# Kernel optimization log

Hardware: AMD Instinct MI355X
Metric: run time of the kernel (lower is better)

The kernel has to match this reference:

```python
import jax, jax.numpy as jnp
import numpy as np

DIM = 1024
N_HEADS = 16
HEAD_DIM = DIM // N_HEADS


def setup_inputs() -> dict:
    key = jax.random.key(0)
    ks = jax.random.split(key, 9)
    s = 0.02
    return {
        "x": jax.random.normal(ks[0], (2, 2048, DIM), dtype=jnp.float32),
        "Wq": jax.random.normal(ks[1], (DIM, DIM), dtype=jnp.float32) * s,
        "bq": jax.random.normal(ks[2], (DIM,), dtype=jnp.float32) * s,
        "Wk": jax.random.normal(ks[3], (DIM, DIM), dtype=jnp.float32) * s,
        "bk": jax.random.normal(ks[4], (DIM,), dtype=jnp.float32) * s,
        "Wv": jax.random.normal(ks[5], (DIM, DIM), dtype=jnp.float32) * s,
        "bv": jax.random.normal(ks[6], (DIM,), dtype=jnp.float32) * s,
        "Wo": jax.random.normal(ks[7], (DIM, DIM), dtype=jnp.float32) * s,
        "bo": jax.random.normal(ks[8], (DIM,), dtype=jnp.float32) * s,
    }


def reference(x, Wq, bq, Wk, bk, Wv, bv, Wo, bo):
    B, T, C = x.shape
    # QKV projections, split heads -> [B, H, T, D]
    def split_heads(t):
        return t.reshape(B, T, N_HEADS, HEAD_DIM).transpose(0, 2, 1, 3)
    q = split_heads(x @ Wq + bq)
    k = split_heads(x @ Wk + bk)
    v = split_heads(x @ Wv + bv)
    scale = 1.0 / jnp.sqrt(jnp.float32(HEAD_DIM))
    scores = jnp.einsum("bhqd,bhkd->bhqk", q, k) * scale  # [B,H,T,T]
    causal = jnp.tril(jnp.ones((T, T), dtype=bool))  # True = keep
    scores = jnp.where(causal, scores, jnp.float32(-jnp.inf))
    weights = jax.nn.softmax(scores, axis=-1)
    ctx = jnp.einsum("bhqk,bhkd->bhqd", weights, v)
    ctx = ctx.transpose(0, 2, 1, 3).reshape(B, T, C)
    return ctx @ Wo + bo
```

## Files before the change

kernel.cpp:

```cpp
#include <hip/hip_runtime.h>
#include <hip/hip_bf16.h>
#include <stdint.h>

#define DIM    1024
#define SEQ    2048
#define NB     2
#define NH     16
#define HD     64
#define NROWS  (NB*SEQ)

typedef unsigned short u16;
typedef __attribute__((ext_vector_type(8))) short bf16x8;
typedef __attribute__((ext_vector_type(4))) float f32x4;
typedef __attribute__((ext_vector_type(4))) unsigned short u16x4;

#define NEG_INF (-__builtin_inff())

__device__ __forceinline__ u16 f2bf(float f) {
    union { float f; uint32_t u; } x; x.f = f;
    uint32_t r = x.u + 0x7FFFu + ((x.u >> 16) & 1u);
    return (u16)(r >> 16);
}

__device__ __forceinline__ void gload_lds16(const void* g, void* l) {
    __builtin_amdgcn_global_load_lds(
        (const __attribute__((address_space(1))) void*)g,
        (__attribute__((address_space(3))) void*)l, 16, 0, 0);
}

__global__ __launch_bounds__(256)
void cvt_x(const float* __restrict__ in, u16* __restrict__ out)
{
    size_t i = (size_t)blockIdx.x * 256 + threadIdx.x;
    float4 f = *(const float4*)&in[i * 4];
    u16x4 o = { f2bf(f.x), f2bf(f.y), f2bf(f.z), f2bf(f.w) };
    *(u16x4*)&out[i * 4] = o;
}

__global__ __launch_bounds__(256)
void cvt_w(const float* __restrict__ Wq, const float* __restrict__ Wk,
           const float* __restrict__ Wv, const float* __restrict__ Wo,
           u16* __restrict__ Wqt, u16* __restrict__ Wkt,
           u16* __restrict__ Wvt, u16* __restrict__ Wot)
{
    __shared__ u16 Ws[64][68];
    const int z = blockIdx.z;
    const float* W = z == 0 ? Wq : z == 1 ? Wk : z == 2 ? Wv : Wo;
    u16* Wt        = z == 0 ? Wqt : z == 1 ? Wkt : z == 2 ? Wvt : Wot;
    const int k0 = blockIdx.x * 64;
    const int n0 = blockIdx.y * 64;
    const int tid = threadIdx.x;

    #pragma unroll
    for (int it = 0; it < 4; ++it) {
        int idx = tid + it * 256;
        int r = idx >> 4, cq = idx & 15;
        float4 f = *(const float4*)&W[(size_t)(k0 + r) * DIM + n0 + cq * 4];
        u16x4 o = { f2bf(f.x), f2bf(f.y), f2bf(f.z), f2bf(f.w) };
        *(u16x4*)&Ws[r][cq * 4] = o;
    }
    __syncthreads();
    #pragma unroll
    for (int it = 0; it < 4; ++it) {
        int idx = tid + it * 256;
        int rr = idx >> 4, cq = idx & 15;
        u16x4 o = { Ws[cq*4+0][rr], Ws[cq*4+1][rr], Ws[cq*4+2][rr], Ws[cq*4+3][rr] };
        *(u16x4*)&Wt[(size_t)(n0 + rr) * DIM + k0 + cq * 4] = o;
    }
}

template<int MODE>
__global__ __launch_bounds__(256)
void gemm_mfma(const u16* __restrict__ A,
               const u16* __restrict__ Wt0, const u16* __restrict__ Wt1,
               const u16* __restrict__ Wt2,
               const float* __restrict__ b0, const float* __restrict__ b1,
               const float* __restrict__ b2,
               void* __restrict__ o0, void* __restrict__ o1, void* __restrict__ o2)
{
    __shared__ __align__(16) uint8_t lds[32768];
    uint8_t* Asb = lds;
    uint8_t* Bsb = lds + 16384;

    const int tid  = threadIdx.x;
    const int wid  = tid >> 6, lane = tid & 63;
    const int lr   = lane & 15, lg = lane >> 4;
    const int wr   = wid >> 1, wc = wid & 1;

    const int r0 = blockIdx.x * 128;
    const int c0 = blockIdx.y * 128;

    const u16* Wt; const float* bias; u16* obf = nullptr; float* ofp = nullptr;
    int cw;
    if (MODE == 0) {
        int sel = c0 >> 10;
        cw  = c0 & 1023;
        Wt   = sel == 0 ? Wt0 : sel == 1 ? Wt1 : Wt2;
        bias = sel == 0 ? b0  : sel == 1 ? b1  : b2;
        obf  = (u16*)(sel == 0 ? o0 : sel == 1 ? o1 : o2);
    } else {
        cw = c0; Wt = Wt0; bias = b0; ofp = (float*)o0;
    }

    f32x4 acc[4][4] = {};

    for (int k0 = 0; k0 < DIM; k0 += 64) {
        __syncthreads();
        #pragma unroll
        for (int seg = 0; seg < 4; ++seg) {
            int o   = seg * 4096 + tid * 16;
            int row = o >> 7;
            int sch = ((o >> 4) & 7) ^ (row & 7);
            gload_lds16((const uint8_t*)A  + ((size_t)(r0 + row) << 11) + (k0 << 1) + (sch << 4),
                        Asb + seg * 4096 + (wid << 10) + (lane << 4));
            gload_lds16((const uint8_t*)Wt + ((size_t)(cw + row) << 11) + (k0 << 1) + (sch << 4),
                        Bsb + seg * 4096 + (wid << 10) + (lane << 4));
        }
        __syncthreads();

        __builtin_amdgcn_s_setprio(1);
        #pragma unroll
        for (int kk = 0; kk < 2; ++kk) {
            bf16x8 a[4], b[4];
            #pragma unroll
            for (int i = 0; i < 4; ++i) {
                int ar = wr * 64 + i * 16 + lr;
                a[i] = *(const bf16x8*)(Asb + ar * 128 + ((((kk << 2) | lg) ^ (ar & 7)) << 4));
                int br = wc * 64 + i * 16 + lr;
                b[i] = *(const bf16x8*)(Bsb + br * 128 + ((((kk << 2) | lg) ^ (br & 7)) << 4));
            }
            #pragma unroll
            for (int i = 0; i < 4; ++i)
                #pragma unroll
                for (int j = 0; j < 4; ++j)
                    acc[i][j] = __builtin_amdgcn_mfma_f32_16x16x32_bf16(a[i], b[j], acc[i][j], 0, 0, 0);
        }
        __builtin_amdgcn_s_setprio(0);
    }

    #pragma unroll
    for (int j = 0; j < 4; ++j) {
        int colw = wc * 64 + j * 16 + lr;
        float bv = bias[cw + colw];
        #pragma unroll
        for (int i = 0; i < 4; ++i) {
            #pragma unroll
            for (int r = 0; r < 4; ++r) {
                float val = acc[i][j][r] + bv;
                int row = r0 + wr * 64 + i * 16 + lg * 4 + r;
                if (MODE == 0) {
                    int col = cw + colw;
                    int h = col >> 6, d = col & 63;
                    int bb = row >> 11, t = row & (SEQ - 1);
                    obf[((((size_t)bb * NH + h) * SEQ + t) << 6) + d] = f2bf(val);
                } else {
                    ofp[((size_t)row << 10) + c0 + colw] = val;
                }
            }
        }
    }
}

__global__ __launch_bounds__(256)
void attn_mfma(const u16* __restrict__ q, const u16* __restrict__ k,
               const u16* __restrict__ v, u16* __restrict__ ctx)
{
    __shared__ __align__(16) uint8_t lds[32768];
    uint8_t* Qs = lds;
    uint8_t* Ks = lds + 8192;
    uint8_t* Vt = lds + 16384;
    uint8_t* Ps = lds + 24576;

    const int tid = threadIdx.x;
    const int wid = tid >> 6, lane = tid & 63;
    const int lr  = lane & 15, lg = lane >> 4;

    const int n  = blockIdx.x;
    const int j4 = n >> 8;
    const int c  = n & 255;
    const int ch = c >> 5;
    const int bh = c & 31;
    const int qt = (j4 == 0) ? ch : (j4 == 1) ? (15 - ch)
                 : (j4 == 2) ? (16 + ch) : (31 - ch);

    const size_t hb = (size_t)bh * SEQ * HD;
    const int q0 = qt * 64;

    #pragma unroll
    for (int seg = 0; seg < 2; ++seg) {
        int o = seg * 4096 + tid * 16;
        int row = o >> 7;
        int sch = ((o >> 4) & 7) ^ (row & 7);
        gload_lds16((const uint8_t*)(q + hb) + (size_t)(q0 + row) * 128 + (sch << 4),
                    Qs + seg * 4096 + (wid << 10) + (lane << 4));
    }

    const int vp = tid >> 3;
    const int vg = tid & 7;

    f32x4 acc[4] = {};
    float mrow[4] = {NEG_INF, NEG_INF, NEG_INF, NEG_INF};
    float lrow[4] = {0.f, 0.f, 0.f, 0.f};
    bf16x8 aQ0, aQ1;

    for (int kt = 0; kt <= qt; ++kt) {
        __syncthreads();
        #pragma unroll
        for (int seg = 0; seg < 2; ++seg) {
            int o = seg * 4096 + tid * 16;
            int row = o >> 7;
            int sch = ((o >> 4) & 7) ^ (row & 7);
            gload_lds16((const uint8_t*)(k + hb) + (size_t)(kt * 64 + row) * 128 + (sch << 4),
                        Ks + seg * 4096 + (wid << 10) + (lane << 4));
        }
        {
            const u16* vsrc = v + hb + ((size_t)(kt * 64 + 2 * vp) << 6) + vg * 8;
            bf16x8 v0 = *(const bf16x8*)vsrc;
            bf16x8 v1 = *(const bf16x8*)(vsrc + 64);
            #pragma unroll
            for (int i = 0; i < 8; ++i) {
                int d = vg * 8 + i;
                int swzd = (d ^ (d >> 3)) & 7;
                uint32_t w = (uint32_t)(u16)v0[i] | ((uint32_t)(u16)v1[i] << 16);
                *(uint32_t*)(Vt + d * 128 + ((((vp >> 2) ^ swzd) << 4)) + ((vp & 3) << 2)) = w;
            }
        }
        __syncthreads();

        if (kt == 0) {
            int qr = wid * 16 + lr;
            aQ0 = *(const bf16x8*)(Qs + qr * 128 + ((lg       ^ (qr & 7)) << 4));
            aQ1 = *(const bf16x8*)(Qs + qr * 128 + (((4 | lg) ^ (qr & 7)) << 4));
        }

        f32x4 s[4];
        __builtin_amdgcn_s_setprio(1);
        #pragma unroll
        for (int j = 0; j < 4; ++j) {
            int krow = j * 16 + lr;
            bf16x8 b0 = *(const bf16x8*)(Ks + krow * 128 + ((lg       ^ (krow & 7)) << 4));
            bf16x8 b1 = *(const bf16x8*)(Ks + krow * 128 + (((4 | lg) ^ (krow & 7)) << 4));
            f32x4 z = {0.f, 0.f, 0.f, 0.f};
            z    = __builtin_amdgcn_mfma_f32_16x16x32_bf16(aQ0, b0, z, 0, 0, 0);
            s[j] = __builtin_amdgcn_mfma_f32_16x16x32_bf16(aQ1, b1, z, 0, 0, 0);
        }
        __builtin_amdgcn_s_setprio(0);

        #pragma unroll
        for (int j = 0; j < 4; ++j)
            #pragma unroll
            for (int r = 0; r < 4; ++r)
                s[j][r] *= 0.125f;
        if (kt == qt) {
            #pragma unroll
            for (int j = 0; j < 4; ++j) {
                int kcol = j * 16 + lr;
                #pragma unroll
                for (int r = 0; r < 4; ++r)
                    if (kcol > wid * 16 + lg * 4 + r) s[j][r] = NEG_INF;
            }
        }

        float alpha[4];
        #pragma unroll
        for (int r = 0; r < 4; ++r) {
            float rm = fmaxf(fmaxf(s[0][r], s[1][r]), fmaxf(s[2][r], s[3][r]));
            rm = fmaxf(rm, __shfl_xor(rm, 1));
            rm = fmaxf(rm, __shfl_xor(rm, 2));
            rm = fmaxf(rm, __shfl_xor(rm, 4));
            rm = fmaxf(rm, __shfl_xor(rm, 8));
            float mn = fmaxf(mrow[r], rm);
            alpha[r] = __expf(mrow[r] - mn);
            mrow[r] = mn;
        }
        float rs[4] = {0.f, 0.f, 0.f, 0.f};
        #pragma unroll
        for (int j = 0; j < 4; ++j)
            #pragma unroll
            for (int r = 0; r < 4; ++r) {
                float p = __expf(s[j][r] - mrow[r]);
                s[j][r] = p;
                rs[r] += p;
            }
        #pragma unroll
        for (int r = 0; r < 4; ++r) {
            float t = rs[r];
            t += __shfl_xor(t, 1);
            t += __shfl_xor(t, 2);
            t += __shfl_xor(t, 4);
            t += __shfl_xor(t, 8);
            lrow[r] = lrow[r] * alpha[r] + t;
        }

        #pragma unroll
        for (int j = 0; j < 4; ++j)
            #pragma unroll
            for (int r = 0; r < 4; ++r) {
                int row = wid * 16 + lg * 4 + r;
                int swzp = (row ^ (row >> 2)) & 7;
                int col = j * 16 + lr;
                *(u16*)(Ps + row * 128 + ((((col >> 3) ^ swzp) << 4)) + ((col & 7) << 1))
                    = f2bf(s[j][r]);
            }

        #pragma unroll
        for (int ni = 0; ni < 4; ++ni)
            #pragma unroll
            for (int r = 0; r < 4; ++r)
                acc[ni][r] *= alpha[r];

        int prow = wid * 16 + lr;
        int swzq = (prow ^ (prow >> 2)) & 7;
        bf16x8 pa0 = *(const bf16x8*)(Ps + prow * 128 + ((lg       ^ swzq) << 4));
        bf16x8 pa1 = *(const bf16x8*)(Ps + prow * 128 + (((4 | lg) ^ swzq) << 4));
        __builtin_amdgcn_s_setprio(1);
        #pragma unroll
        for (int ni = 0; ni < 4; ++ni) {
            int vrow = ni * 16 + lr;
            int swzd = (vrow ^ (vrow >> 3)) & 7;
            bf16x8 vb0 = *(const bf16x8*)(Vt + vrow * 128 + ((lg       ^ swzd) << 4));
            bf16x8 vb1 = *(const bf16x8*)(Vt + vrow * 128 + (((4 | lg) ^ swzd) << 4));
            acc[ni] = __builtin_amdgcn_mfma_f32_16x16x32_bf16(pa0, vb0, acc[ni], 0, 0, 0);
            acc[ni] = __builtin_amdgcn_mfma_f32_16x16x32_bf16(pa1, vb1, acc[ni], 0, 0, 0);
        }
        __builtin_amdgcn_s_setprio(0);
    }

    const int b = bh >> 4, h = bh & 15;
    #pragma unroll
    for (int r = 0; r < 4; ++r) {
        float rl = 1.f / lrow[r];
        int t = q0 + wid * 16 + lg * 4 + r;
        size_t base = (((size_t)b * SEQ + t) << 10) + (h << 6);
        #pragma unroll
        for (int ni = 0; ni < 4; ++ni)
            ctx[base + ni * 16 + lr] = f2bf(acc[ni][r] * rl);
    }
}

extern "C" void kernel_launch(void* const* d_in, const int* in_sizes, int n_in,
                              void* d_out, int out_size, void* d_ws, size_t ws_size,
                              hipStream_t stream)
{
    (void)in_sizes; (void)n_in; (void)out_size; (void)ws_size;
    const float* x  = (const float*)d_in[0];
    const float* Wq = (const float*)d_in[1];
    const float* bq = (const float*)d_in[2];
    const float* Wk = (const float*)d_in[3];
    const float* bk = (const float*)d_in[4];
    const float* Wv = (const float*)d_in[5];
    const float* bv = (const float*)d_in[6];
    const float* Wo = (const float*)d_in[7];
    const float* bo = (const float*)d_in[8];

    u16* ws = (u16*)d_ws;
    const size_t M1 = (size_t)1024 * 1024;
    const size_t M4 = (size_t)NROWS * DIM;
    u16* xb  = ws;
    u16* wqt = ws + M4;
    u16* wkt = wqt + M1;
    u16* wvt = wkt + M1;
    u16* wot = wvt + M1;
    u16* qb  = wot + M1;
    u16* kb  = qb + M4;
    u16* vb  = kb + M4;
    u16* cb  = vb + M4;

    cvt_x<<<dim3(4096), dim3(256), 0, stream>>>(x, xb);
    cvt_w<<<dim3(16, 16, 4), dim3(256), 0, stream>>>(Wq, Wk, Wv, Wo, wqt, wkt, wvt, wot);
    gemm_mfma<0><<<dim3(32, 24), dim3(256), 0, stream>>>(
        xb, wqt, wkt, wvt, bq, bk, bv, qb, kb, vb);
    attn_mfma<<<dim3(1024), dim3(256), 0, stream>>>(qb, kb, vb, cb);
    gemm_mfma<1><<<dim3(32, 8), dim3(256), 0, stream>>>(
        cb, wot, nullptr, nullptr, bo, nullptr, nullptr, d_out, nullptr, nullptr);
}
```

Measured before the change: 211.5 us.

## Keep softmax probabilities in registers via transposed QK^T MFMA and permuted V layout

The attention kernel now computes S transposed (K as the A operand), so each lane holds one query row's scores. That lets the row max and sum reduce with two cross-lane shuffles, and the probabilities feed the PV MFMA directly from registers instead of being written to and reread from an LDS P buffer. V is stored in LDS with a permuted key ordering to match the register layout of P. The 1/sqrt(d) scale is folded into the Q projection epilogue. This removes the LDS round trip, the per-element scale multiply and most shuffles, at the cost of extra shuffles to broadcast alpha and 1/l, and a trickier layout to keep correct.

```diff
diff --git a/kernel.cpp b/kernel.cpp
--- a/kernel.cpp
+++ b/kernel.cpp
@@ -91,13 +91,14 @@
     const int c0 = blockIdx.y * 128;
 
     const u16* Wt; const float* bias; u16* obf = nullptr; float* ofp = nullptr;
-    int cw;
+    int cw; float qscale = 1.0f;
     if (MODE == 0) {
         int sel = c0 >> 10;
         cw  = c0 & 1023;
         Wt   = sel == 0 ? Wt0 : sel == 1 ? Wt1 : Wt2;
         bias = sel == 0 ? b0  : sel == 1 ? b1  : b2;
         obf  = (u16*)(sel == 0 ? o0 : sel == 1 ? o1 : o2);
+        if (sel == 0) qscale = 0.125f;
     } else {
         cw = c0; Wt = Wt0; bias = b0; ofp = (float*)o0;
     }
@@ -146,7 +147,7 @@
         for (int i = 0; i < 4; ++i) {
             #pragma unroll
             for (int r = 0; r < 4; ++r) {
-                float val = acc[i][j][r] + bv;
+                float val = (acc[i][j][r] + bv) * qscale;
                 int row = r0 + wr * 64 + i * 16 + lg * 4 + r;
                 if (MODE == 0) {
                     int col = cw + colw;
@@ -165,11 +166,10 @@
 void attn_mfma(const u16* __restrict__ q, const u16* __restrict__ k,
                const u16* __restrict__ v, u16* __restrict__ ctx)
 {
-    __shared__ __align__(16) uint8_t lds[32768];
+    __shared__ __align__(16) uint8_t lds[24576];
     uint8_t* Qs = lds;
     uint8_t* Ks = lds + 8192;
     uint8_t* Vt = lds + 16384;
-    uint8_t* Ps = lds + 24576;
 
     const int tid = threadIdx.x;
     const int wid = tid >> 6, lane = tid & 63;
@@ -197,10 +197,14 @@
 
     const int vp = tid >> 3;
     const int vg = tid & 7;
+    const int vj  = vp >> 3;
+    const int vlg = (vp >> 1) & 3;
+    const int vrr = (vp & 1) * 2;
+    const int vslot = (vj & 1) * 32 + vlg * 8 + ((vj >> 1) << 2) + vrr;
 
     f32x4 acc[4] = {};
-    float mrow[4] = {NEG_INF, NEG_INF, NEG_INF, NEG_INF};
-    float lrow[4] = {0.f, 0.f, 0.f, 0.f};
+    float m_own = NEG_INF;
+    float l_own = 0.f;
     bf16x8 aQ0, aQ1;
 
     for (int kt = 0; kt <= qt; ++kt) {
@@ -222,7 +226,8 @@
                 int d = vg * 8 + i;
                 int swzd = (d ^ (d >> 3)) & 7;
                 uint32_t w = (uint32_t)(u16)v0[i] | ((uint32_t)(u16)v1[i] << 16);
-                *(uint32_t*)(Vt + d * 128 + ((((vp >> 2) ^ swzd) << 4)) + ((vp & 3) << 2)) = w;
+                *(uint32_t*)(Vt + d * 128 + ((((vslot >> 3) ^ swzd) << 4))
+                             + ((vslot & 7) << 1)) = w;
             }
         }
         __syncthreads();
@@ -241,78 +246,62 @@
             bf16x8 b0 = *(const bf16x8*)(Ks + krow * 128 + ((lg       ^ (krow & 7)) << 4));
             bf16x8 b1 = *(const bf16x8*)(Ks + krow * 128 + (((4 | lg) ^ (krow & 7)) << 4));
             f32x4 z = {0.f, 0.f, 0.f, 0.f};
-            z    = __builtin_amdgcn_mfma_f32_16x16x32_bf16(aQ0, b0, z, 0, 0, 0);
-            s[j] = __builtin_amdgcn_mfma_f32_16x16x32_bf16(aQ1, b1, z, 0, 0, 0);
+            z    = __builtin_amdgcn_mfma_f32_16x16x32_bf16(b0, aQ0, z, 0, 0, 0);
+            s[j] = __builtin_amdgcn_mfma_f32_16x16x32_bf16(b1, aQ1, z, 0, 0, 0);
         }
         __builtin_amdgcn_s_setprio(0);
 
-        #pragma unroll
-        for (int j = 0; j < 4; ++j)
-            #pragma unroll
-            for (int r = 0; r < 4; ++r)
-                s[j][r] *= 0.125f;
         if (kt == qt) {
             #pragma unroll
-            for (int j = 0; j < 4; ++j) {
-                int kcol = j * 16 + lr;
+            for (int j = 0; j < 4; ++j)
                 #pragma unroll
                 for (int r = 0; r < 4; ++r)
-                    if (kcol > wid * 16 + lg * 4 + r) s[j][r] = NEG_INF;
+                    if (j * 16 + lg * 4 + r > wid * 16 + lr) s[j][r] = NEG_INF;
+        }
+
+        float rm = NEG_INF;
+        #pragma unroll
+        for (int j = 0; j < 4; ++j) {
+            float a = fmaxf(fmaxf(s[j][0], s[j][1]), fmaxf(s[j][2], s[j][3]));
+            rm = fmaxf(rm, a);
+        }
+        rm = fmaxf(rm, __shfl_xor(rm, 16));
+        rm = fmaxf(rm, __shfl_xor(rm, 32));
+        float mnew = fmaxf(m_own, rm);
+        float aown = __expf(m_own - mnew);
+        m_own = mnew;
+
+        float rs = 0.f;
+        #pragma unroll
+        for (int j = 0; j < 4; ++j)
+            #pragma unroll
+            for (int r = 0; r < 4; ++r) {
+                float p = __expf(s[j][r] - mnew);
+                s[j][r] = p;
+                rs += p;
             }
-        }
-
-        float alpha[4];
-        #pragma unroll
-        for (int r = 0; r < 4; ++r) {
-            float rm = fmaxf(fmaxf(s[0][r], s[1][r]), fmaxf(s[2][r], s[3][r]));
-            rm = fmaxf(rm, __shfl_xor(rm, 1));
-            rm = fmaxf(rm, __shfl_xor(rm, 2));
-            rm = fmaxf(rm, __shfl_xor(rm, 4));
-            rm = fmaxf(rm, __shfl_xor(rm, 8));
-            float mn = fmaxf(mrow[r], rm);
-            alpha[r] = __expf(mrow[r] - mn);
-            mrow[r] = mn;
-        }
-        float rs[4] = {0.f, 0.f, 0.f, 0.f};
-        #pragma unroll
-        for (int j = 0; j < 4; ++j)
-            #pragma unroll
-            for (int r = 0; r < 4; ++r) {
-                float p = __expf(s[j][r] - mrow[r]);
-                s[j][r] = p;
-                rs[r] += p;
-            }
-        #pragma unroll
-        for (int r = 0; r < 4; ++r) {
-            float t = rs[r];
-            t += __shfl_xor(t, 1);
-            t += __shfl_xor(t, 2);
-            t += __shfl_xor(t, 4);
-            t += __shfl_xor(t, 8);
-            lrow[r] = lrow[r] * alpha[r] + t;
-        }
-
-        #pragma unroll
-        for (int j = 0; j < 4; ++j)
-            #pragma unroll
-            for (int r = 0; r < 4; ++r) {
-                int row = wid * 16 + lg * 4 + r;
-                int swzp = (row ^ (row >> 2)) & 7;
-                int col = j * 16 + lr;
-                *(u16*)(Ps + row * 128 + ((((col >> 3) ^ swzp) << 4)) + ((col & 7) << 1))
-                    = f2bf(s[j][r]);
-            }
-
+        rs += __shfl_xor(rs, 16);
+        rs += __shfl_xor(rs, 32);
+        l_own = l_own * aown + rs;
+
+        float ar[4];
+        #pragma unroll
+        for (int r = 0; r < 4; ++r) ar[r] = __shfl(aown, lg * 4 + r);
         #pragma unroll
         for (int ni = 0; ni < 4; ++ni)
             #pragma unroll
             for (int r = 0; r < 4; ++r)
-                acc[ni][r] *= alpha[r];
-
-        int prow = wid * 16 + lr;
-        int swzq = (prow ^ (prow >> 2)) & 7;
-        bf16x8 pa0 = *(const bf16x8*)(Ps + prow * 128 + ((lg       ^ swzq) << 4));
-        bf16x8 pa1 = *(const bf16x8*)(Ps + prow * 128 + (((4 | lg) ^ swzq) << 4));
+                acc[ni][r] *= ar[r];
+
+        bf16x8 pa0, pa1;
+        #pragma unroll
+        for (int i = 0; i < 4; ++i) {
+            pa0[i]     = (short)f2bf(s[0][i]);
+            pa0[4 + i] = (short)f2bf(s[2][i]);
+            pa1[i]     = (short)f2bf(s[1][i]);
+            pa1[4 + i] = (short)f2bf(s[3][i]);
+        }
+
         __builtin_amdgcn_s_setprio(1);
         #pragma unroll
         for (int ni = 0; ni < 4; ++ni) {
@@ -326,15 +315,19 @@
         __builtin_amdgcn_s_setprio(0);
     }
 
+    float rinv = 1.f / l_own;
+    float rl[4];
+    #pragma unroll
+    for (int r = 0; r < 4; ++r) rl[r] = __shfl(rinv, lg * 4 + r);
+
     const int b = bh >> 4, h = bh & 15;
     #pragma unroll
     for (int r = 0; r < 4; ++r) {
-        float rl = 1.f / lrow[r];
         int t = q0 + wid * 16 + lg * 4 + r;
         size_t base = (((size_t)b * SEQ + t) << 10) + (h << 6);
         #pragma unroll
         for (int ni = 0; ni < 4; ++ni)
-            ctx[base + ni * 16 + lr] = f2bf(acc[ni][r] * rl);
+            ctx[base + ni * 16 + lr] = f2bf(acc[ni][r] * rl[r]);
     }
 }
 
```

Measured after the change: 190.8 us. 1.11x faster.
